# Optimization experiments

Measured on AMD Instinct MI355X. Metric: run time of the kernel, lower is better.

The kernel has to match this reference:

```python
import jax, jax.numpy as jnp
import numpy as np

N = 50000
E = 800000
F_IN = 128
HID = 64
HEADS = 4
P = 16384


def setup_inputs() -> dict:
    key = jax.random.key(0)
    ks = jax.random.split(key, 20)
    s = 0.05
    inp = {
        'x': jax.random.normal(ks[0], (N, F_IN), jnp.float32),
        'edge_src': jax.random.randint(ks[1], (E,), 0, N, jnp.int32),
        'edge_dst': jax.random.randint(ks[2], (E,), 0, N, jnp.int32),
        'edge_attr': jax.random.uniform(ks[3], (E, 1), jnp.float32),
        'pair_indices': jax.random.randint(ks[4], (P, 2), 0, N, jnp.int32),
        # conv1: in=F_IN, heads=4, out=HID, edge_dim=1
        'W1': jax.random.normal(ks[5], (F_IN, HEADS * HID), jnp.float32) * s,
        'We1': jax.random.normal(ks[6], (1, HEADS * HID), jnp.float32) * s,
        'as1': jax.random.normal(ks[7], (HEADS, HID), jnp.float32) * s,
        'ad1': jax.random.normal(ks[8], (HEADS, HID), jnp.float32) * s,
        'ae1': jax.random.normal(ks[9], (HEADS, HID), jnp.float32) * s,
        'b1': jnp.zeros((HEADS * HID,), jnp.float32),
        # conv2: in=4*HID, heads=1, out=HID
        'W2': jax.random.normal(ks[10], (HEADS * HID, HID), jnp.float32) * s,
        'We2': jax.random.normal(ks[11], (1, HID), jnp.float32) * s,
        'as2': jax.random.normal(ks[12], (1, HID), jnp.float32) * s,
        'ad2': jax.random.normal(ks[13], (1, HID), jnp.float32) * s,
        'ae2': jax.random.normal(ks[14], (1, HID), jnp.float32) * s,
        'b2': jnp.zeros((HID,), jnp.float32),
        'Wlin': jax.random.normal(ks[15], (2 * HID, 1), jnp.float32) * s,
        'blin': jnp.zeros((1,), jnp.float32),
    }
    return inp


def gat_conv(x, src, dst, edge_attr, W, We, att_src, att_dst, att_edge, bias, heads, C):
    """PyG GATConv (add_self_loops=True, fill_value='mean', negative_slope=0.2, eval mode)."""
    n = x.shape[0]
    # self-loop edge_attr = mean of incoming edge attrs per node
    deg = jax.ops.segment_sum(jnp.ones_like(dst, dtype=edge_attr.dtype), dst, num_segments=n)
    loop_attr = jax.ops.segment_sum(edge_attr, dst, num_segments=n) / jnp.maximum(deg, 1.0)[:, None]
    loop = jnp.arange(n, dtype=src.dtype)
    src_f = jnp.concatenate([src, loop])
    dst_f = jnp.concatenate([dst, loop])
    ea = jnp.concatenate([edge_attr, loop_attr], axis=0)  # [E+N, 1]
    h = (x @ W).reshape(n, heads, C)                      # [N, H, C]
    a_src = (h * att_src).sum(-1)                         # [N, H]
    a_dst = (h * att_dst).sum(-1)
    e = (ea @ We).reshape(-1, heads, C)                   # [E+N, H, C]
    a_edge = (e * att_edge).sum(-1)                       # [E+N, H]
    alpha = jax.nn.leaky_relu(a_src[src_f] + a_dst[dst_f] + a_edge, 0.2)
    amax = jax.ops.segment_max(alpha, dst_f, num_segments=n)
    ex = jnp.exp(alpha - amax[dst_f])
    denom = jax.ops.segment_sum(ex, dst_f, num_segments=n)
    w = ex / denom[dst_f]                                 # segment softmax over dst
    msg = h[src_f] * w[..., None]                         # [E+N, H, C]
    out = jax.ops.segment_sum(msg, dst_f, num_segments=n) # [N, H, C]
    return out.reshape(n, heads * C) + bias


def reference(x, edge_src, edge_dst, edge_attr, pair_indices,
              W1, We1, as1, ad1, ae1, b1,
              W2, We2, as2, ad2, ae2, b2, Wlin, blin):
    # dropout is identity in eval mode
    h1 = jax.nn.elu(gat_conv(x, edge_src, edge_dst, edge_attr,
                             W1, We1, as1, ad1, ae1, b1, HEADS, HID))
    h2 = gat_conv(h1, edge_src, edge_dst, edge_attr,
                  W2, We2, as2, ad2, ae2, b2, 1, HID)
    d1 = h2[pair_indices[:, 0]]
    d2 = h2[pair_indices[:, 1]]
    pf = jnp.concatenate([d1, d2], axis=1)                # [P, 2*HID]
    return jax.nn.sigmoid(pf @ Wlin + blin).reshape(-1)
```

## Files before the change

### kernel.cpp

```cpp
#include <hip/hip_runtime.h>
#include <hip/hip_fp16.h>
#include <math.h>

typedef __attribute__((ext_vector_type(8))) short short8;
typedef __attribute__((ext_vector_type(4))) float floatx4;
typedef __attribute__((ext_vector_type(2))) float float2v;

#define LOG2E 1.4426950408889634f

__device__ __forceinline__ unsigned short f2bf(float f){
  unsigned int x = __float_as_uint(f);
  unsigned int r = x + 0x7fff + ((x >> 16) & 1);
  return (unsigned short)(r >> 16);
}
__device__ __forceinline__ unsigned cvtpkbf(float lo, float hi){
  unsigned r;
  asm("v_cvt_pk_bf16_f32 %0, %1, %2" : "=v"(r) : "v"(lo), "v"(hi));
  return r;
}
__device__ __forceinline__ short8 pk8(float4 a0, float4 a1){
  unsigned t[4];
  t[0] = cvtpkbf(a0.x, a0.y); t[1] = cvtpkbf(a0.z, a0.w);
  t[2] = cvtpkbf(a1.x, a1.y); t[3] = cvtpkbf(a1.z, a1.w);
  short8 r; __builtin_memcpy(&r, t, 16); return r;
}
__device__ __forceinline__ unsigned char f2fp8(float v){
  int pk = __builtin_amdgcn_cvt_pk_fp8_f32(v, 0.f, 0, false);
  return (unsigned char)(pk & 0xff);
}
__device__ __forceinline__ float wsumf(float v){
#pragma unroll
  for (int o = 32; o; o >>= 1) v += __shfl_xor(v, o, 64);
  return v;
}
__device__ __forceinline__ unsigned pkh2(float a, float b){
  auto p = __builtin_amdgcn_cvt_pkrtz(a, b);
  unsigned u; __builtin_memcpy(&u, &p, 4); return u;
}
__device__ __forceinline__ float h2f(unsigned v){
  unsigned short us = (unsigned short)v;
  __fp16 h; __builtin_memcpy(&h, &us, 2);
  return (float)h;
}

__global__ __launch_bounds__(256) void k_count_prep(const int* __restrict__ dst,
    const float* __restrict__ eattr, unsigned* __restrict__ degp,
    unsigned char* __restrict__ rank, int E, int N, int ebl2,
    const float* __restrict__ W1, const float* __restrict__ as1,
    const float* __restrict__ ad1, const float* __restrict__ W2,
    const float* __restrict__ as2, const float* __restrict__ ad2,
    const float* __restrict__ We1, const float* __restrict__ ae1,
    const float* __restrict__ We2, const float* __restrict__ ae2,
    const float* __restrict__ b2, const float* __restrict__ Wlin,
    unsigned short* __restrict__ W1p, float* __restrict__ w2vT,
    float* __restrict__ ce){
  if ((int)blockIdx.x < ebl2){
    int e0 = blockIdx.x * 512 + threadIdx.x;
    int e1 = e0 + 256;
    bool v0 = e0 < E, v1 = e1 < E;
    int d0 = 0, d1 = 0; float a0 = 0.f, a1 = 0.f;
    if (v0){ d0 = dst[e0]; a0 = eattr[e0]; }
    if (v1){ d1 = dst[e1]; a1 = eattr[e1]; }
    int b0 = (e0 >> 8) & 7, b1 = (e1 >> 8) & 7;
    if (v0){
      unsigned old = atomicAdd(&degp[(size_t)b0 * N + d0],
                               (1u << 24) | (unsigned)(a0 * 262144.0f));
      rank[e0] = (unsigned char)(old >> 24);
    }
    if (v1){
      unsigned old = atomicAdd(&degp[(size_t)b1 * N + d1],
                               (1u << 24) | (unsigned)(a1 * 262144.0f));
      rank[e1] = (unsigned char)(old >> 24);
    }
    return;
  }
  if (threadIdx.x >= 64) return;
  int b = blockIdx.x - ebl2, lane = threadIdx.x;
  if (b < 68){
    int nt = b >> 2, kc = b & 3;
    int col = lane & 15, krow = kc * 32 + (lane >> 4) * 8;
    unsigned short tmp[8];
    if (nt < 16){
#pragma unroll
      for (int j = 0; j < 8; j++) tmp[j] = f2bf(W1[(size_t)(krow + j) * 256 + nt * 16 + col]);
    } else {
#pragma unroll
      for (int j = 0; j < 8; j++){
        float v = 0.f;
        if (col < 8){
          const float* av = (col < 4) ? as1 : ad1;
          int h = col & 3;
          for (int c = 0; c < 64; c++)
            v += W1[(size_t)(krow + j) * 256 + h * 64 + c] * av[h * 64 + c];
          v *= LOG2E;
        }
        tmp[j] = f2bf(v);
      }
    }
    unsigned short* dstp = W1p + (((size_t)nt * 4 + kc) * 64 + lane) * 8;
    *(ushort4*)(dstp)     = make_ushort4(tmp[0], tmp[1], tmp[2], tmp[3]);
    *(ushort4*)(dstp + 4) = make_ushort4(tmp[4], tmp[5], tmp[6], tmp[7]);
  } else if (b < 72){
    int k = (b - 68) * 64 + lane;
    float4 a = make_float4(0.f, 0.f, 0.f, 0.f);
    for (int c = 0; c < 64; c++){
      float wv = W2[(size_t)k * 64 + c];
      a.x += wv * as2[c];
      a.y += wv * ad2[c];
      a.z += wv * Wlin[c];
      a.w += wv * Wlin[64 + c];
    }
    w2vT[k]       = a.x * LOG2E;
    w2vT[256 + k] = a.y * LOG2E;
    w2vT[512 + k] = a.z;
    w2vT[768 + k] = a.w;
  } else {
    float p0 = We1[lane]       * ae1[lane];
    float p1 = We1[64 + lane]  * ae1[64 + lane];
    float p2 = We1[128 + lane] * ae1[128 + lane];
    float p3 = We1[192 + lane] * ae1[192 + lane];
    float p4 = We2[lane]       * ae2[lane];
    float c1 = b2[lane] * Wlin[lane];
    float c2 = b2[lane] * Wlin[64 + lane];
    p0 = wsumf(p0); p1 = wsumf(p1); p2 = wsumf(p2); p3 = wsumf(p3); p4 = wsumf(p4);
    c1 = wsumf(c1); c2 = wsumf(c2);
    if (lane == 0){
      ce[0] = p0 * LOG2E; ce[1] = p1 * LOG2E; ce[2] = p2 * LOG2E; ce[3] = p3 * LOG2E;
      ce[4] = p4 * LOG2E;
      ce[5] = c1; ce[6] = c2;
    }
  }
}

__global__ __launch_bounds__(256, 2) void k_scan1_gemm(
    const unsigned* __restrict__ degp, int* __restrict__ row_ptr,
    int* __restrict__ bsum, int n, int gbl,
    const float* __restrict__ A, const unsigned short* __restrict__ Bp,
    unsigned char* __restrict__ h1f8, float* __restrict__ asrc,
    float* __restrict__ adst, int M){
  __shared__ unsigned short Bs[256 * 128];
  if ((int)blockIdx.x >= gbl){
    int* sm = (int*)Bs;
    int sb = blockIdx.x - gbl;
    int tid = threadIdx.x, gid = sb * 256 + tid;
    int v = 0;
    if (gid < n){
#pragma unroll
      for (int b = 0; b < 8; b++) v += (int)(degp[(size_t)b * n + gid] >> 24);
    }
    sm[tid] = v; __syncthreads();
    int pin = 0;
    for (int off = 1; off < 256; off <<= 1){
      int t = sm[pin * 256 + tid];
      if (tid >= off) t += sm[pin * 256 + tid - off];
      sm[(pin ^ 1) * 256 + tid] = t; pin ^= 1; __syncthreads();
    }
    int incl = sm[pin * 256 + tid];
    if (gid < n) row_ptr[gid] = incl - v;
    if (tid == 255) bsum[sb] = incl;
    return;
  }
  constexpr int K = 128, NKC = 4;
  {
    const uint4* srcp = (const uint4*)Bp;
    uint4* dstp = (uint4*)Bs;
    for (int i = threadIdx.x; i < 4096; i += 256) dstp[i] = srcp[i];
  }
  __syncthreads();
  int wave = threadIdx.x >> 6, lane = threadIdx.x & 63;
  int quad = lane >> 4, col = lane & 15;
  int r0a = blockIdx.x * 128 + wave * 16;
  int r0b = r0a + 64;
  int rowa = min(r0a + col, M - 1);
  int rowb = min(r0b + col, M - 1);
  short8 afa[NKC], afb[NKC], sf[NKC];
#pragma unroll
  for (int kc = 0; kc < NKC; kc++){
    float4 a0 = *(const float4*)(A + (size_t)rowa * K + kc * 32 + quad * 8);
    float4 a1 = *(const float4*)(A + (size_t)rowa * K + kc * 32 + quad * 8 + 4);
    float4 b0 = *(const float4*)(A + (size_t)rowb * K + kc * 32 + quad * 8);
    float4 b1 = *(const float4*)(A + (size_t)rowb * K + kc * 32 + quad * 8 + 4);
    afa[kc] = pk8(a0, a1);
    afb[kc] = pk8(b0, b1);
    sf[kc] = *(const short8*)(Bp + (((size_t)16 * 4 + kc) * 64 + lane) * 8);
  }
  floatx4 acc0[17], acc1[17];
#pragma unroll
  for (int nt = 0; nt < 17; nt++){
    acc0[nt] = (floatx4){0.f, 0.f, 0.f, 0.f};
    acc1[nt] = (floatx4){0.f, 0.f, 0.f, 0.f};
  }
#pragma unroll
  for (int kc = 0; kc < NKC; kc++){
#pragma unroll
    for (int nt = 0; nt < 16; nt++){
      short8 bfv = *(const short8*)(&Bs[((nt * NKC + kc) * 64 + lane) * 8]);
      acc0[nt] = __builtin_amdgcn_mfma_f32_16x16x32_bf16(afa[kc], bfv, acc0[nt], 0, 0, 0);
      acc1[nt] = __builtin_amdgcn_mfma_f32_16x16x32_bf16(afb[kc], bfv, acc1[nt], 0, 0, 0);
    }
    acc0[16] = __builtin_amdgcn_mfma_f32_16x16x32_bf16(afa[kc], sf[kc], acc0[16], 0, 0, 0);
    acc1[16] = __builtin_amdgcn_mfma_f32_16x16x32_bf16(afb[kc], sf[kc], acc1[16], 0, 0, 0);
  }
#pragma unroll
  for (int nt = 0; nt < 16; nt++){
#pragma unroll
    for (int i = 0; i < 4; i++){
      int r = r0a + quad * 4 + i;
      if (r < M) h1f8[(size_t)r * 256 + nt * 16 + col] = f2fp8(acc0[nt][i]);
    }
  }
#pragma unroll
  for (int i = 0; i < 4; i++){
    int r = r0a + quad * 4 + i;
    if (r < M){
      float v = acc0[16][i];
      if (col < 4)      asrc[(size_t)r * 4 + col] = v;
      else if (col < 8) adst[(size_t)r * 4 + (col - 4)] = v;
    }
  }
#pragma unroll
  for (int nt = 0; nt < 16; nt++){
#pragma unroll
    for (int i = 0; i < 4; i++){
      int r = r0b + quad * 4 + i;
      if (r < M) h1f8[(size_t)r * 256 + nt * 16 + col] = f2fp8(acc1[nt][i]);
    }
  }
#pragma unroll
  for (int i = 0; i < 4; i++){
    int r = r0b + quad * 4 + i;
    if (r < M){
      float v = acc1[16][i];
      if (col < 4)      asrc[(size_t)r * 4 + col] = v;
      else if (col < 8) adst[(size_t)r * 4 + (col - 4)] = v;
    }
  }
}

__global__ __launch_bounds__(256) void k_scan3(int* __restrict__ row_ptr,
    const int* __restrict__ bsum, const unsigned* __restrict__ degp,
    float* __restrict__ lattr, int* __restrict__ base, int n, int E){
  int tid = threadIdx.x;
  int partial = (tid < (int)blockIdx.x) ? bsum[tid] : 0;
#pragma unroll
  for (int o = 32; o; o >>= 1) partial += __shfl_xor(partial, o, 64);
  __shared__ int ws[4];
  if ((tid & 63) == 0) ws[tid >> 6] = partial;
  __syncthreads();
  int blockOfs = ws[0] + ws[1] + ws[2] + ws[3];
  int gid = blockIdx.x * 256 + tid;
  if (gid >= n) return;
  int rp = row_ptr[gid] + blockOfs;
  row_ptr[gid] = rp;
  int cum = 0; float s = 0.f;
  int bb[8];
#pragma unroll
  for (int b = 0; b < 8; b++){
    unsigned p = degp[(size_t)b * n + gid];
    bb[b] = rp + cum;
    cum += (int)(p >> 24);
    s += (float)(p & 0xffffffu);
  }
  lattr[gid] = (s * (1.0f / 262144.0f)) / fmaxf((float)cum, 1.0f);
  int4* bp = (int4*)(base + (size_t)gid * 8);
  bp[0] = make_int4(bb[0], bb[1], bb[2], bb[3]);
  bp[1] = make_int4(bb[4], bb[5], bb[6], bb[7]);
  if (gid == 0) row_ptr[n] = E;
}

__global__ __launch_bounds__(256) void k_scatter(const int* __restrict__ src,
    const int* __restrict__ dst, const float* __restrict__ eattr,
    const unsigned char* __restrict__ rank, const int* __restrict__ base,
    const float* __restrict__ a_src, int4* __restrict__ csr, int E){
  int e0 = blockIdx.x * 512 + threadIdx.x;
  int e1 = e0 + 256;
  bool v0 = e0 < E, v1 = e1 < E;
  int b0 = (e0 >> 8) & 7, b1 = (e1 >> 8) & 7;
  if (v0){
    int d = dst[e0], s = src[e0];
    int pos = base[(size_t)d * 8 + b0] + (int)rank[e0];
    float4 av = *(const float4*)(a_src + ((size_t)s << 2));
    csr[pos] = make_int4(s, __float_as_int(eattr[e0]),
                         (int)pkh2(av.x, av.y), (int)pkh2(av.z, av.w));
  }
  if (v1){
    int d = dst[e1], s = src[e1];
    int pos = base[(size_t)d * 8 + b1] + (int)rank[e1];
    float4 av = *(const float4*)(a_src + ((size_t)s << 2));
    csr[pos] = make_int4(s, __float_as_int(eattr[e1]),
                         (int)pkh2(av.x, av.y), (int)pkh2(av.z, av.w));
  }
}

__global__ __launch_bounds__(128) void k_gat1(
    const int* __restrict__ row_ptr, const int4* __restrict__ csr,
    const float* __restrict__ lattr,
    const float* __restrict__ a_src, const float* __restrict__ a_dst,
    const float* __restrict__ ce, const unsigned char* __restrict__ hpre,
    const float* __restrict__ bias, const float* __restrict__ w2vT,
    float4* __restrict__ upd, int n){
  int node = blockIdx.x * 2 + (threadIdx.x >> 6);
  if (node >= n) return;
  int lane = threadIdx.x & 63;
  int q = lane >> 4, lsub = lane & 15, hq = lsub >> 2;
  int start = row_ptr[node], deg = row_ptr[node + 1] - start;
  float4 as4 = *(const float4*)(a_src + (size_t)node * 4);
  float4 ad4 = *(const float4*)(a_dst + (size_t)node * 4);
  float4 ce4 = *(const float4*)ce;
  float la = lattr[node];
  float asvh = hq == 0 ? as4.x : hq == 1 ? as4.y : hq == 2 ? as4.z : as4.w;
  float advh = hq == 0 ? ad4.x : hq == 1 ? ad4.y : hq == 2 ? ad4.z : ad4.w;
  float ceh  = hq == 0 ? ce4.x : hq == 1 ? ce4.y : hq == 2 ? ce4.z : ce4.w;
  unsigned lso = (unsigned)(lsub << 4);
  int hsh = (hq & 1) * 16;
  float2v acc2[8];
#pragma unroll
  for (int k = 0; k < 8; k++) acc2[k] = (float2v){0.f, 0.f};
  float dn = 0.f;
  if (q == 0){
    float aself = fmaf(la, ceh, asvh + advh);
    aself = aself > 0.f ? aself : 0.2f * aself;
    float wself = __builtin_amdgcn_exp2f(aself);
    dn = wself;
    uint4 u = *(const uint4*)(hpre + (((unsigned)node << 8) + lso));
    float2v w2 = (float2v){wself, wself};
    unsigned uu[4] = {u.x, u.y, u.z, u.w};
#pragma unroll
    for (int j = 0; j < 4; j++){
      acc2[2 * j]     = w2 * __builtin_amdgcn_cvt_pk_f32_fp8((int)uu[j], false);
      acc2[2 * j + 1] = w2 * __builtin_amdgcn_cvt_pk_f32_fp8((int)uu[j], true);
    }
  }
  for (int e = q; e < deg; e += 8){
    bool vB = (e + 4) < deg;
    int4 sA = csr[start + e];
    int4 sB = csr[start + (vB ? e + 4 : e)];
    uint4 uA = *(const uint4*)(hpre + (((unsigned)sA.x << 8) + lso));
    uint4 uB = *(const uint4*)(hpre + (((unsigned)sB.x << 8) + lso));
    unsigned hwA = (hq & 2) ? (unsigned)sA.w : (unsigned)sA.z;
    unsigned hwB = (hq & 2) ? (unsigned)sB.w : (unsigned)sB.z;
    float gA = h2f(hwA >> hsh);
    float gB = h2f(hwB >> hsh);
    float aA = fmaf(__int_as_float(sA.y), ceh, gA + advh);
    float aB = fmaf(__int_as_float(sB.y), ceh, gB + advh);
    aA = aA > 0.f ? aA : 0.2f * aA;
    aB = aB > 0.f ? aB : 0.2f * aB;
    float wA = __builtin_amdgcn_exp2f(aA);
    float wB = vB ? __builtin_amdgcn_exp2f(aB) : 0.f;
    dn += wA + wB;
    float2v wA2 = (float2v){wA, wA}, wB2 = (float2v){wB, wB};
    unsigned ua[4] = {uA.x, uA.y, uA.z, uA.w};
    unsigned ub[4] = {uB.x, uB.y, uB.z, uB.w};
#pragma unroll
    for (int j = 0; j < 4; j++){
      acc2[2 * j]     += wA2 * __builtin_amdgcn_cvt_pk_f32_fp8((int)ua[j], false);
      acc2[2 * j + 1] += wA2 * __builtin_amdgcn_cvt_pk_f32_fp8((int)ua[j], true);
      acc2[2 * j]     += wB2 * __builtin_amdgcn_cvt_pk_f32_fp8((int)ub[j], false);
      acc2[2 * j + 1] += wB2 * __builtin_amdgcn_cvt_pk_f32_fp8((int)ub[j], true);
    }
  }
  dn += __shfl_xor(dn, 16, 64);
  dn += __shfl_xor(dn, 32, 64);
#pragma unroll
  for (int k = 0; k < 8; k++){
    acc2[k].x += __shfl_xor(acc2[k].x, 16, 64);
    acc2[k].x += __shfl_xor(acc2[k].x, 32, 64);
    acc2[k].y += __shfl_xor(acc2[k].y, 16, 64);
    acc2[k].y += __shfl_xor(acc2[k].y, 32, 64);
  }
  {
    float inv = 1.f / dn;
    float d = 0.f;
#pragma unroll
    for (int j = 0; j < 4; j++){
      float4 b4  = *(const float4*)(bias + lsub * 16 + j * 4);
      float4 wvj = *(const float4*)(w2vT + (size_t)lane * 16 + j * 4);
      float bbv[4] = {b4.x, b4.y, b4.z, b4.w};
      float wvv[4] = {wvj.x, wvj.y, wvj.z, wvj.w};
#pragma unroll
      for (int t = 0; t < 4; t++){
        int k = j * 4 + t;
        float av = (k & 1) ? acc2[k >> 1].y : acc2[k >> 1].x;
        float v = av * inv + bbv[t];
        v = v > 0.f ? v : (__expf(v) - 1.f);
        d += v * wvv[t];
      }
    }
#pragma unroll
    for (int o = 1; o < 16; o <<= 1) d += __shfl_xor(d, o, 64);
    if (lsub == 0) ((float*)&upd[node])[q] = d;
  }
}

__global__ __launch_bounds__(128) void k_gat2(
    const int* __restrict__ row_ptr, const int4* __restrict__ csr,
    const float* __restrict__ lattr, const float4* __restrict__ upd,
    const float* __restrict__ ce,
    float* __restrict__ s1v, float* __restrict__ s2v, int n){
  int node = blockIdx.x * 16 + (threadIdx.x >> 3);
  if (node >= n) return;
  int lane8 = threadIdx.x & 7;
  int start = row_ptr[node], deg = row_ptr[node + 1] - start;
  float4 own = upd[node];
  float ad = own.y, c = ce[4];
  const float* updf = (const float*)upd;
  float t1 = 0.f, t2 = 0.f, dn = 0.f;
  if (lane8 == 0){
    float a = fmaf(lattr[node], c, own.x + ad);
    a = a > 0.f ? a : 0.2f * a;
    float w = __builtin_amdgcn_exp2f(a);
    dn = w; t1 = w * own.z; t2 = w * own.w;
  }
  for (int e = lane8; e < deg; e += 16){
    bool vB = (e + 8) < deg;
    int4 sA = csr[start + e];
    int4 sB = csr[start + (vB ? e + 8 : e)];
    float4 oA = *(const float4*)(updf + ((unsigned)sA.x << 2));
    float4 oB = *(const float4*)(updf + ((unsigned)sB.x << 2));
    float aA = fmaf(__int_as_float(sA.y), c, oA.x + ad);
    float aB = fmaf(__int_as_float(sB.y), c, oB.x + ad);
    aA = aA > 0.f ? aA : 0.2f * aA;
    aB = aB > 0.f ? aB : 0.2f * aB;
    float wA = __builtin_amdgcn_exp2f(aA);
    float wB = vB ? __builtin_amdgcn_exp2f(aB) : 0.f;
    dn += wA + wB;
    t1 = fmaf(wA, oA.z, fmaf(wB, oB.z, t1));
    t2 = fmaf(wA, oA.w, fmaf(wB, oB.w, t2));
  }
#pragma unroll
  for (int o = 1; o < 8; o <<= 1){
    dn += __shfl_xor(dn, o, 64);
    t1 += __shfl_xor(t1, o, 64);
    t2 += __shfl_xor(t2, o, 64);
  }
  if (lane8 == 0){
    float inv = 1.f / dn;
    s1v[node] = t1 * inv + ce[5];
    s2v[node] = t2 * inv + ce[6];
  }
}

__global__ __launch_bounds__(256) void k_pairs(const int* __restrict__ pairs,
    const float* __restrict__ s1v, const float* __restrict__ s2v,
    const float* __restrict__ blin, float* __restrict__ out, int P){
  int p = blockIdx.x * 256 + threadIdx.x;
  if (p >= P) return;
  int i = pairs[2 * p], j = pairs[2 * p + 1];
  float x = s1v[i] + s2v[j] + blin[0];
  out[p] = 1.f / (1.f + __expf(-x));
}

extern "C" void kernel_launch(void* const* d_in, const int* in_sizes, int n_in,
                              void* d_out, int out_size, void* d_ws, size_t ws_size,
                              hipStream_t stream) {
  const float* x     = (const float*)d_in[0];
  const int*   esrc  = (const int*)  d_in[1];
  const int*   edst  = (const int*)  d_in[2];
  const float* eattr = (const float*)d_in[3];
  const int*   pairs = (const int*)  d_in[4];
  const float* W1    = (const float*)d_in[5];
  const float* We1   = (const float*)d_in[6];
  const float* as1   = (const float*)d_in[7];
  const float* ad1   = (const float*)d_in[8];
  const float* ae1   = (const float*)d_in[9];
  const float* b1    = (const float*)d_in[10];
  const float* W2    = (const float*)d_in[11];
  const float* We2   = (const float*)d_in[12];
  const float* as2   = (const float*)d_in[13];
  const float* ad2   = (const float*)d_in[14];
  const float* ae2   = (const float*)d_in[15];
  const float* b2    = (const float*)d_in[16];
  const float* Wlin  = (const float*)d_in[17];
  const float* blin  = (const float*)d_in[18];
  float* out = (float*)d_out;

  const int N = in_sizes[0] / 128;
  const int E = in_sizes[1];
  const int P = in_sizes[4] / 2;

  char* w = (char*)d_ws;
  size_t off = 0;
  auto alloc = [&](size_t bytes) -> size_t {
    size_t r = off; off = (off + bytes + 255) & ~(size_t)255; return r;
  };
  size_t o_degp   = alloc((size_t)N * 32);
  size_t zero_end = off;
  size_t o_rank   = alloc((size_t)E);
  size_t o_rowptr = alloc((size_t)(N + 1) * 4);
  size_t o_bsum   = alloc(1024);
  size_t o_lattr  = alloc((size_t)N * 4);
  size_t o_base   = alloc((size_t)N * 32);
  size_t o_csr    = alloc((size_t)E * 16);
  size_t o_asrc1  = alloc((size_t)N * 16);
  size_t o_adst1  = alloc((size_t)N * 16);
  size_t o_upd    = alloc((size_t)N * 16);
  size_t o_ce     = alloc(64);
  size_t o_s1     = alloc((size_t)N * 4);
  size_t o_s2     = alloc((size_t)N * 4);
  size_t o_W1p    = alloc((size_t)17 * 4 * 64 * 8 * 2);
  size_t o_w2v    = alloc(256 * 16);
  size_t o_h1f8   = alloc((size_t)N * 256);
  (void)ws_size;

  unsigned* degp = (unsigned*)(w + o_degp);
  unsigned char* rank = (unsigned char*)(w + o_rank);
  int*   rowptr = (int*)  (w + o_rowptr);
  int*   bsum   = (int*)  (w + o_bsum);
  float* lattr  = (float*)(w + o_lattr);
  int*   base   = (int*)  (w + o_base);
  int4*  csr    = (int4*) (w + o_csr);
  float* asrc1  = (float*)(w + o_asrc1);
  float* adst1  = (float*)(w + o_adst1);
  float4* upd   = (float4*)(w + o_upd);
  float* ce     = (float*)(w + o_ce);
  float* s1v    = (float*)(w + o_s1);
  float* s2v    = (float*)(w + o_s2);
  unsigned short* W1p = (unsigned short*)(w + o_W1p);
  float* w2vT   = (float*)(w + o_w2v);
  unsigned char* h1f8 = (unsigned char*)(w + o_h1f8);

  (void)hipMemsetAsync(w, 0, zero_end, stream);

  int ebl2 = (E + 511) / 512;
  int nbl = (N + 255) / 256;
  int gbl = (N + 127) / 128;
  int wbl = (N + 1) / 2;

  k_count_prep<<<ebl2 + 73, 256, 0, stream>>>(edst, eattr, degp, rank, E, N, ebl2,
      W1, as1, ad1, W2, as2, ad2, We1, ae1, We2, ae2, b2, Wlin, W1p, w2vT, ce);
  k_scan1_gemm<<<gbl + nbl, 256, 0, stream>>>(degp, rowptr, bsum, N, gbl,
      x, W1p, h1f8, asrc1, adst1, N);
  k_scan3<<<nbl, 256, 0, stream>>>(rowptr, bsum, degp, lattr, base, N, E);
  k_scatter<<<ebl2, 256, 0, stream>>>(esrc, edst, eattr, rank, base, asrc1, csr, E);
  k_gat1<<<wbl, 128, 0, stream>>>(rowptr, csr, lattr, asrc1, adst1, ce,
                                  h1f8, b1, w2vT, upd, N);
  k_gat2<<<(N + 15) / 16, 128, 0, stream>>>(rowptr, csr, lattr, upd, ce,
                                            s1v, s2v, N);
  k_pairs<<<(P + 255) / 256, 256, 0, stream>>>(pairs, s1v, s2v, blin, out, P);
}
```

Measured before the change: 247.5 us.

## Replace stored edge ranks with scatter-time atomics and prefetch CSR entries in gat1

The counting pass no longer returns the old atomic value or writes a per-edge rank byte array. The scatter kernel instead claims slots with an atomicAdd on the per-destination bucket base, so the count atomics become fire-and-forget and the rank buffer traffic disappears. Separately, the gat1 edge loop now loads the next iteration's CSR entries before processing the current ones, to overlap the dependent csr-to-hpre load chain. The cost is a second set of atomics during scatter, and edge order within a bucket becomes nondeterministic, which can slightly change floating-point summation order.

```diff
diff --git a/kernel.cpp b/kernel.cpp
--- a/kernel.cpp
+++ b/kernel.cpp
@@ -45,7 +45,7 @@
 
 __global__ __launch_bounds__(256) void k_count_prep(const int* __restrict__ dst,
     const float* __restrict__ eattr, unsigned* __restrict__ degp,
-    unsigned char* __restrict__ rank, int E, int N, int ebl2,
+    int E, int N, int ebl2,
     const float* __restrict__ W1, const float* __restrict__ as1,
     const float* __restrict__ ad1, const float* __restrict__ W2,
     const float* __restrict__ as2, const float* __restrict__ ad2,
@@ -62,16 +62,10 @@
     if (v0){ d0 = dst[e0]; a0 = eattr[e0]; }
     if (v1){ d1 = dst[e1]; a1 = eattr[e1]; }
     int b0 = (e0 >> 8) & 7, b1 = (e1 >> 8) & 7;
-    if (v0){
-      unsigned old = atomicAdd(&degp[(size_t)b0 * N + d0],
-                               (1u << 24) | (unsigned)(a0 * 262144.0f));
-      rank[e0] = (unsigned char)(old >> 24);
-    }
-    if (v1){
-      unsigned old = atomicAdd(&degp[(size_t)b1 * N + d1],
-                               (1u << 24) | (unsigned)(a1 * 262144.0f));
-      rank[e1] = (unsigned char)(old >> 24);
-    }
+    if (v0) atomicAdd(&degp[(size_t)b0 * N + d0],
+                      (1u << 24) | (unsigned)(a0 * 262144.0f));
+    if (v1) atomicAdd(&degp[(size_t)b1 * N + d1],
+                      (1u << 24) | (unsigned)(a1 * 262144.0f));
     return;
   }
   if (threadIdx.x >= 64) return;
@@ -270,7 +264,7 @@
 
 __global__ __launch_bounds__(256) void k_scatter(const int* __restrict__ src,
     const int* __restrict__ dst, const float* __restrict__ eattr,
-    const unsigned char* __restrict__ rank, const int* __restrict__ base,
+    int* __restrict__ base,
     const float* __restrict__ a_src, int4* __restrict__ csr, int E){
   int e0 = blockIdx.x * 512 + threadIdx.x;
   int e1 = e0 + 256;
@@ -278,14 +272,14 @@
   int b0 = (e0 >> 8) & 7, b1 = (e1 >> 8) & 7;
   if (v0){
     int d = dst[e0], s = src[e0];
-    int pos = base[(size_t)d * 8 + b0] + (int)rank[e0];
+    int pos = atomicAdd(&base[(size_t)d * 8 + b0], 1);
     float4 av = *(const float4*)(a_src + ((size_t)s << 2));
     csr[pos] = make_int4(s, __float_as_int(eattr[e0]),
                          (int)pkh2(av.x, av.y), (int)pkh2(av.z, av.w));
   }
   if (v1){
     int d = dst[e1], s = src[e1];
-    int pos = base[(size_t)d * 8 + b1] + (int)rank[e1];
+    int pos = atomicAdd(&base[(size_t)d * 8 + b1], 1);
     float4 av = *(const float4*)(a_src + ((size_t)s << 2));
     csr[pos] = make_int4(s, __float_as_int(eattr[e1]),
                          (int)pkh2(av.x, av.y), (int)pkh2(av.z, av.w));
@@ -331,12 +325,19 @@
       acc2[2 * j + 1] = w2 * __builtin_amdgcn_cvt_pk_f32_fp8((int)uu[j], true);
     }
   }
+  int4 sA = make_int4(0, 0, 0, 0), sB;
+  if (q < deg) sA = csr[start + q];
+  sB = sA;
+  if (q + 4 < deg) sB = csr[start + q + 4];
   for (int e = q; e < deg; e += 8){
-    bool vB = (e + 4) < deg;
-    int4 sA = csr[start + e];
-    int4 sB = csr[start + (vB ? e + 4 : e)];
     uint4 uA = *(const uint4*)(hpre + (((unsigned)sA.x << 8) + lso));
     uint4 uB = *(const uint4*)(hpre + (((unsigned)sB.x << 8) + lso));
+    int4 nA = sA, nB;
+    int en = e + 8;
+    if (en < deg) nA = csr[start + en];
+    nB = nA;
+    if (en + 4 < deg) nB = csr[start + en + 4];
+    bool vB = (e + 4) < deg;
     unsigned hwA = (hq & 2) ? (unsigned)sA.w : (unsigned)sA.z;
     unsigned hwB = (hq & 2) ? (unsigned)sB.w : (unsigned)sB.z;
     float gA = h2f(hwA >> hsh);
@@ -358,6 +359,7 @@
       acc2[2 * j]     += wB2 * __builtin_amdgcn_cvt_pk_f32_fp8((int)ub[j], false);
       acc2[2 * j + 1] += wB2 * __builtin_amdgcn_cvt_pk_f32_fp8((int)ub[j], true);
     }
+    sA = nA; sB = nB;
   }
   dn += __shfl_xor(dn, 16, 64);
   dn += __shfl_xor(dn, 32, 64);
@@ -485,7 +487,6 @@
   };
   size_t o_degp   = alloc((size_t)N * 32);
   size_t zero_end = off;
-  size_t o_rank   = alloc((size_t)E);
   size_t o_rowptr = alloc((size_t)(N + 1) * 4);
   size_t o_bsum   = alloc(1024);
   size_t o_lattr  = alloc((size_t)N * 4);
@@ -503,7 +504,6 @@
   (void)ws_size;
 
   unsigned* degp = (unsigned*)(w + o_degp);
-  unsigned char* rank = (unsigned char*)(w + o_rank);
   int*   rowptr = (int*)  (w + o_rowptr);
   int*   bsum   = (int*)  (w + o_bsum);
   float* lattr  = (float*)(w + o_lattr);
@@ -526,12 +526,12 @@
   int gbl = (N + 127) / 128;
   int wbl = (N + 1) / 2;
 
-  k_count_prep<<<ebl2 + 73, 256, 0, stream>>>(edst, eattr, degp, rank, E, N, ebl2,
+  k_count_prep<<<ebl2 + 73, 256, 0, stream>>>(edst, eattr, degp, E, N, ebl2,
       W1, as1, ad1, W2, as2, ad2, We1, ae1, We2, ae2, b2, Wlin, W1p, w2vT, ce);
   k_scan1_gemm<<<gbl + nbl, 256, 0, stream>>>(degp, rowptr, bsum, N, gbl,
       x, W1p, h1f8, asrc1, adst1, N);
   k_scan3<<<nbl, 256, 0, stream>>>(rowptr, bsum, degp, lattr, base, N, E);
-  k_scatter<<<ebl2, 256, 0, stream>>>(esrc, edst, eattr, rank, base, asrc1, csr, E);
+  k_scatter<<<ebl2, 256, 0, stream>>>(esrc, edst, eattr, base, asrc1, csr, E);
   k_gat1<<<wbl, 128, 0, stream>>>(rowptr, csr, lattr, asrc1, adst1, ce,
                                   h1f8, b1, w2vT, upd, N);
   k_gat2<<<(N + 15) / 16, 128, 0, stream>>>(rowptr, csr, lattr, upd, ce,
```

New measurement: 269.5 us. +8.9%, slower.

## Overlap edge counting with GEMM, halve GEMM LDS, prefetch CSR in gat1

Applied to the files above, without the earlier changes.

The edge degree-counting atomics move out of the weight-prep kernel and into the same launch as the x@W1 GEMM, so the atomic work runs concurrently with the MFMA blocks. The prefix scan becomes its own kernel. The GEMM now stages the packed B matrix through LDS in two halves, halving shared memory to raise occupancy, at the cost of extra barriers. In gat1 the CSR entries for the next iteration are software-prefetched to hide load latency. The schedule gains one extra kernel launch.

```diff
diff --git a/kernel.cpp b/kernel.cpp
--- a/kernel.cpp
+++ b/kernel.cpp
@@ -43,9 +43,7 @@
   return (float)h;
 }
 
-__global__ __launch_bounds__(256) void k_count_prep(const int* __restrict__ dst,
-    const float* __restrict__ eattr, unsigned* __restrict__ degp,
-    unsigned char* __restrict__ rank, int E, int N, int ebl2,
+__global__ __launch_bounds__(64) void k_prep(
     const float* __restrict__ W1, const float* __restrict__ as1,
     const float* __restrict__ ad1, const float* __restrict__ W2,
     const float* __restrict__ as2, const float* __restrict__ ad2,
@@ -54,28 +52,7 @@
     const float* __restrict__ b2, const float* __restrict__ Wlin,
     unsigned short* __restrict__ W1p, float* __restrict__ w2vT,
     float* __restrict__ ce){
-  if ((int)blockIdx.x < ebl2){
-    int e0 = blockIdx.x * 512 + threadIdx.x;
-    int e1 = e0 + 256;
-    bool v0 = e0 < E, v1 = e1 < E;
-    int d0 = 0, d1 = 0; float a0 = 0.f, a1 = 0.f;
-    if (v0){ d0 = dst[e0]; a0 = eattr[e0]; }
-    if (v1){ d1 = dst[e1]; a1 = eattr[e1]; }
-    int b0 = (e0 >> 8) & 7, b1 = (e1 >> 8) & 7;
-    if (v0){
-      unsigned old = atomicAdd(&degp[(size_t)b0 * N + d0],
-                               (1u << 24) | (unsigned)(a0 * 262144.0f));
-      rank[e0] = (unsigned char)(old >> 24);
-    }
-    if (v1){
-      unsigned old = atomicAdd(&degp[(size_t)b1 * N + d1],
-                               (1u << 24) | (unsigned)(a1 * 262144.0f));
-      rank[e1] = (unsigned char)(old >> 24);
-    }
-    return;
-  }
-  if (threadIdx.x >= 64) return;
-  int b = blockIdx.x - ebl2, lane = threadIdx.x;
+  int b = blockIdx.x, lane = threadIdx.x;
   if (b < 68){
     int nt = b >> 2, kc = b & 3;
     int col = lane & 15, krow = kc * 32 + (lane >> 4) * 8;
@@ -132,41 +109,36 @@
   }
 }
 
-__global__ __launch_bounds__(256, 2) void k_scan1_gemm(
-    const unsigned* __restrict__ degp, int* __restrict__ row_ptr,
-    int* __restrict__ bsum, int n, int gbl,
+__global__ __launch_bounds__(256, 2) void k_count_gemm(
+    const int* __restrict__ dst, const float* __restrict__ eattr,
+    unsigned* __restrict__ degp, unsigned char* __restrict__ rank,
+    int E, int N, int gbl,
     const float* __restrict__ A, const unsigned short* __restrict__ Bp,
     unsigned char* __restrict__ h1f8, float* __restrict__ asrc,
     float* __restrict__ adst, int M){
-  __shared__ unsigned short Bs[256 * 128];
+  __shared__ unsigned short Bs[256 * 64];
   if ((int)blockIdx.x >= gbl){
-    int* sm = (int*)Bs;
-    int sb = blockIdx.x - gbl;
-    int tid = threadIdx.x, gid = sb * 256 + tid;
-    int v = 0;
-    if (gid < n){
-#pragma unroll
-      for (int b = 0; b < 8; b++) v += (int)(degp[(size_t)b * n + gid] >> 24);
-    }
-    sm[tid] = v; __syncthreads();
-    int pin = 0;
-    for (int off = 1; off < 256; off <<= 1){
-      int t = sm[pin * 256 + tid];
-      if (tid >= off) t += sm[pin * 256 + tid - off];
-      sm[(pin ^ 1) * 256 + tid] = t; pin ^= 1; __syncthreads();
-    }
-    int incl = sm[pin * 256 + tid];
-    if (gid < n) row_ptr[gid] = incl - v;
-    if (tid == 255) bsum[sb] = incl;
+    int eb = blockIdx.x - gbl;
+    int e0 = eb * 512 + threadIdx.x;
+    int e1 = e0 + 256;
+    bool v0 = e0 < E, v1 = e1 < E;
+    int d0 = 0, d1 = 0; float a0 = 0.f, a1 = 0.f;
+    if (v0){ d0 = dst[e0]; a0 = eattr[e0]; }
+    if (v1){ d1 = dst[e1]; a1 = eattr[e1]; }
+    int b0 = (e0 >> 8) & 7, b1 = (e1 >> 8) & 7;
+    if (v0){
+      unsigned old = atomicAdd(&degp[(size_t)b0 * N + d0],
+                               (1u << 24) | (unsigned)(a0 * 262144.0f));
+      rank[e0] = (unsigned char)(old >> 24);
+    }
+    if (v1){
+      unsigned old = atomicAdd(&degp[(size_t)b1 * N + d1],
+                               (1u << 24) | (unsigned)(a1 * 262144.0f));
+      rank[e1] = (unsigned char)(old >> 24);
+    }
     return;
   }
   constexpr int K = 128, NKC = 4;
-  {
-    const uint4* srcp = (const uint4*)Bp;
-    uint4* dstp = (uint4*)Bs;
-    for (int i = threadIdx.x; i < 4096; i += 256) dstp[i] = srcp[i];
-  }
-  __syncthreads();
   int wave = threadIdx.x >> 6, lane = threadIdx.x & 63;
   int quad = lane >> 4, col = lane & 15;
   int r0a = blockIdx.x * 128 + wave * 16;
@@ -191,13 +163,26 @@
     acc1[nt] = (floatx4){0.f, 0.f, 0.f, 0.f};
   }
 #pragma unroll
+  for (int ph = 0; ph < 2; ph++){
+    {
+      const uint4* srcp = (const uint4*)(Bp + ph * 16384);
+      uint4* dstp = (uint4*)Bs;
+      for (int i = threadIdx.x; i < 2048; i += 256) dstp[i] = srcp[i];
+    }
+    __syncthreads();
+#pragma unroll
+    for (int kc = 0; kc < NKC; kc++){
+#pragma unroll
+      for (int t = 0; t < 8; t++){
+        short8 bfv = *(const short8*)(&Bs[((t * NKC + kc) * 64 + lane) * 8]);
+        acc0[ph * 8 + t] = __builtin_amdgcn_mfma_f32_16x16x32_bf16(afa[kc], bfv, acc0[ph * 8 + t], 0, 0, 0);
+        acc1[ph * 8 + t] = __builtin_amdgcn_mfma_f32_16x16x32_bf16(afb[kc], bfv, acc1[ph * 8 + t], 0, 0, 0);
+      }
+    }
+    __syncthreads();
+  }
+#pragma unroll
   for (int kc = 0; kc < NKC; kc++){
-#pragma unroll
-    for (int nt = 0; nt < 16; nt++){
-      short8 bfv = *(const short8*)(&Bs[((nt * NKC + kc) * 64 + lane) * 8]);
-      acc0[nt] = __builtin_amdgcn_mfma_f32_16x16x32_bf16(afa[kc], bfv, acc0[nt], 0, 0, 0);
-      acc1[nt] = __builtin_amdgcn_mfma_f32_16x16x32_bf16(afb[kc], bfv, acc1[nt], 0, 0, 0);
-    }
     acc0[16] = __builtin_amdgcn_mfma_f32_16x16x32_bf16(afa[kc], sf[kc], acc0[16], 0, 0, 0);
     acc1[16] = __builtin_amdgcn_mfma_f32_16x16x32_bf16(afb[kc], sf[kc], acc1[16], 0, 0, 0);
   }
@@ -235,6 +220,27 @@
       else if (col < 8) adst[(size_t)r * 4 + (col - 4)] = v;
     }
   }
+}
+
+__global__ __launch_bounds__(256) void k_scan1(const unsigned* __restrict__ degp,
+    int* __restrict__ row_ptr, int* __restrict__ bsum, int n){
+  __shared__ int sm[2][256];
+  int tid = threadIdx.x, gid = blockIdx.x * 256 + tid;
+  int v = 0;
+  if (gid < n){
+#pragma unroll
+    for (int b = 0; b < 8; b++) v += (int)(degp[(size_t)b * n + gid] >> 24);
+  }
+  sm[0][tid] = v; __syncthreads();
+  int pin = 0;
+  for (int off = 1; off < 256; off <<= 1){
+    int t = sm[pin][tid];
+    if (tid >= off) t += sm[pin][tid - off];
+    sm[pin ^ 1][tid] = t; pin ^= 1; __syncthreads();
+  }
+  int incl = sm[pin][tid];
+  if (gid < n) row_ptr[gid] = incl - v;
+  if (tid == 255) bsum[blockIdx.x] = incl;
 }
 
 __global__ __launch_bounds__(256) void k_scan3(int* __restrict__ row_ptr,
@@ -331,12 +337,19 @@
       acc2[2 * j + 1] = w2 * __builtin_amdgcn_cvt_pk_f32_fp8((int)uu[j], true);
     }
   }
+  int4 sA = make_int4(0, 0, 0, 0), sB;
+  if (q < deg) sA = csr[start + q];
+  sB = sA;
+  if (q + 4 < deg) sB = csr[start + q + 4];
   for (int e = q; e < deg; e += 8){
-    bool vB = (e + 4) < deg;
-    int4 sA = csr[start + e];
-    int4 sB = csr[start + (vB ? e + 4 : e)];
     uint4 uA = *(const uint4*)(hpre + (((unsigned)sA.x << 8) + lso));
     uint4 uB = *(const uint4*)(hpre + (((unsigned)sB.x << 8) + lso));
+    int4 nA = sA, nB;
+    int en = e + 8;
+    if (en < deg) nA = csr[start + en];
+    nB = nA;
+    if (en + 4 < deg) nB = csr[start + en + 4];
+    bool vB = (e + 4) < deg;
     unsigned hwA = (hq & 2) ? (unsigned)sA.w : (unsigned)sA.z;
     unsigned hwB = (hq & 2) ? (unsigned)sB.w : (unsigned)sB.z;
     float gA = h2f(hwA >> hsh);
@@ -358,6 +371,7 @@
       acc2[2 * j]     += wB2 * __builtin_amdgcn_cvt_pk_f32_fp8((int)ub[j], false);
       acc2[2 * j + 1] += wB2 * __builtin_amdgcn_cvt_pk_f32_fp8((int)ub[j], true);
     }
+    sA = nA; sB = nB;
   }
   dn += __shfl_xor(dn, 16, 64);
   dn += __shfl_xor(dn, 32, 64);
@@ -526,10 +540,11 @@
   int gbl = (N + 127) / 128;
   int wbl = (N + 1) / 2;
 
-  k_count_prep<<<ebl2 + 73, 256, 0, stream>>>(edst, eattr, degp, rank, E, N, ebl2,
-      W1, as1, ad1, W2, as2, ad2, We1, ae1, We2, ae2, b2, Wlin, W1p, w2vT, ce);
-  k_scan1_gemm<<<gbl + nbl, 256, 0, stream>>>(degp, rowptr, bsum, N, gbl,
+  k_prep<<<73, 64, 0, stream>>>(W1, as1, ad1, W2, as2, ad2,
+                                We1, ae1, We2, ae2, b2, Wlin, W1p, w2vT, ce);
+  k_count_gemm<<<gbl + ebl2, 256, 0, stream>>>(edst, eattr, degp, rank, E, N, gbl,
       x, W1p, h1f8, asrc1, adst1, N);
+  k_scan1<<<nbl, 256, 0, stream>>>(degp, rowptr, bsum, N);
   k_scan3<<<nbl, 256, 0, stream>>>(rowptr, bsum, degp, lattr, base, N, E);
   k_scatter<<<ebl2, 256, 0, stream>>>(esrc, edst, eattr, rank, base, asrc1, csr, E);
   k_gat1<<<wbl, 128, 0, stream>>>(rowptr, csr, lattr, asrc1, adst1, ce,
```

Result: faster. 237.1 us (-4.2%).
